# Kernel optimization log

Hardware: AMD Instinct MI355X
Metric: run time of the kernel (lower is better)

The kernel has to match this reference:

```python
import jax, jax.numpy as jnp
import numpy as np

B = 16384          # batch
F = 26             # num sparse features
D = 13             # num dense features
V = 100000         # vocab per sparse feature
E = 16             # embedding size
HID = [400, 400, 400]
DNN_IN = F * E + D  # 429


def setup_inputs() -> dict:
    key = jax.random.key(0)
    ks = jax.random.split(key, 16)
    inp = {}
    inp["x_sparse"] = jax.random.randint(ks[0], (B, F), 0, V, dtype=jnp.int32)
    inp["x_dense"] = jax.random.uniform(ks[1], (B, D), dtype=jnp.float32)
    # embedding tables (stacked across features; all vocabs equal)
    inp["emb1"] = jax.random.normal(ks[2], (F, V, 1), dtype=jnp.float32) * 0.0001
    inp["emb2"] = jax.random.normal(ks[3], (F, V, E), dtype=jnp.float32) * 0.0001
    inp["w_dense"] = jax.random.normal(ks[4], (D, 1), dtype=jnp.float32) * 0.0001
    inp["bias"] = jnp.zeros((1,), dtype=jnp.float32)
    dims = [DNN_IN] + HID
    for i in range(3):
        inp[f"dnn_w{i}"] = jax.random.normal(ks[5 + i], (dims[i], dims[i + 1]), dtype=jnp.float32) * 0.02
        inp[f"dnn_b{i}"] = jnp.zeros((dims[i + 1],), dtype=jnp.float32)
    inp["final_w"] = jax.random.normal(ks[9], (HID[-1], 1), dtype=jnp.float32) * 0.02
    return inp


def reference(x_sparse, x_dense, emb1, emb2, w_dense, bias,
              dnn_w0, dnn_b0, dnn_w1, dnn_b1, dnn_w2, dnn_b2, final_w):
    f_idx = jnp.arange(F)[None, :]                      # [1, F]
    # FM linear: per-feature 1-d embedding lookup, summed over features
    e1 = emb1[f_idx, x_sparse, 0]                       # [B, F]
    linear_sparse = jnp.sum(e1, axis=-1, keepdims=True)  # [B, 1]
    linear_dense = x_dense @ w_dense                    # [B, 1]
    logit = linear_sparse + linear_dense
    # FM second order: square-of-sum minus sum-of-square
    fm = emb2[f_idx, x_sparse]                          # [B, F, E]
    s = jnp.sum(fm, axis=1)                             # [B, E]
    cross = 0.5 * jnp.sum(s * s - jnp.sum(fm * fm, axis=1), axis=-1, keepdims=True)  # [B, 1]
    logit = logit + cross
    # DNN
    h = jnp.concatenate([fm.reshape(x_sparse.shape[0], F * E), x_dense], axis=-1)  # [B, F*E+D]
    h = jax.nn.relu(h @ dnn_w0 + dnn_b0)
    h = jax.nn.relu(h @ dnn_w1 + dnn_b1)
    h = jax.nn.relu(h @ dnn_w2 + dnn_b2)
    logit = logit + h @ final_w                         # [B, 1]
    return jax.nn.sigmoid(logit + bias)
```

## Files before the change

kernel.cpp:

```cpp
#include <hip/hip_runtime.h>
#include <hip/hip_bf16.h>
#include <math.h>

#define BATCH 16384
#define NF 26
#define ND 13
#define VOC 100000
#define KP0 448
#define KP1 416
#define CS 80
#define NSL 5
#define NGB 4096

typedef __bf16 bf16x8 __attribute__((ext_vector_type(8)));
typedef float f32x4 __attribute__((ext_vector_type(4)));
using bf16 = __hip_bfloat16;
typedef unsigned short u16;

__device__ __forceinline__ void gload_lds16(const void* g, void* l) {
  __builtin_amdgcn_global_load_lds(
      (const __attribute__((address_space(1))) void*)g,
      (__attribute__((address_space(3))) void*)l, 16, 0, 0);
}

__device__ __forceinline__ u16 f2bu(float v) {
  union { __hip_bfloat16 b; u16 u; } cv;
  cv.b = __float2bfloat16(v);
  return cv.u;
}

__global__ __launch_bounds__(256) void prep_gather_kernel(
    const float* __restrict__ w0, const float* __restrict__ w1,
    const float* __restrict__ w2, bf16* __restrict__ wt0,
    bf16* __restrict__ wt1, bf16* __restrict__ wt2,
    const int* __restrict__ xs, const float* __restrict__ xd,
    const float* __restrict__ emb1, const float* __restrict__ emb2,
    const float* __restrict__ wd, const float* __restrict__ biasp,
    bf16* __restrict__ h0, float* __restrict__ partial) {
  const int bid = blockIdx.x, tid = threadIdx.x;
  if (bid >= NGB) {
    const int pbid = bid - NGB;
    const float* W; bf16* Wt; int K, KP, idx;
    if (pbid < 728)       { W = w0; Wt = wt0; K = 429; KP = KP0; idx = pbid * 256 + tid; }
    else if (pbid < 1404) { W = w1; Wt = wt1; K = 400; KP = KP1; idx = (pbid - 728) * 256 + tid; }
    else                  { W = w2; Wt = wt2; K = 400; KP = KP1; idx = (pbid - 1404) * 256 + tid; }
    int k = idx % KP, n = idx / KP;
    float v = (k < K && n < 400) ? W[(size_t)k * 400 + n] : 0.f;
    Wt[idx] = __float2bfloat16(v);
    return;
  }
  const int p = bid;
  const int x8 = p & 7, qb = p >> 3;
  const int gl = (qb >> 5) * 256 + x8 * 32 + (qb & 31);
  const int w = tid >> 6, lane = tid & 63;
  const int b = gl * 4 + w;
  const int q = lane >> 2, sub = lane & 3;

  int xsl = 0;
  if (lane < NF) xsl = xs[b * NF + lane];
  float lin = 0.f;
  if (lane < NF) lin = emb1[(size_t)lane * VOC + xsl];
  if (lane < ND) lin += xd[b * ND + lane] * wd[lane];

  float4 sv = make_float4(0.f, 0.f, 0.f, 0.f);
  float sq = 0.f;
#pragma unroll
  for (int i = 0; i < 2; ++i) {
    int f = i * 16 + q;
    if (f < NF) {
      int idx = __shfl(xsl, f);
      float4 v = *((const float4*)(emb2 + ((size_t)f * VOC + idx) * 16) + sub);
      sv.x += v.x; sv.y += v.y; sv.z += v.z; sv.w += v.w;
      sq += v.x * v.x + v.y * v.y + v.z * v.z + v.w * v.w;
      ushort4 st;
      st.x = f2bu(v.x); st.y = f2bu(v.y); st.z = f2bu(v.z); st.w = f2bu(v.w);
      *(ushort4*)(h0 + (size_t)b * KP0 + f * 16 + sub * 4) = st;
    }
  }
  if (lane < 32) {
    float v = (lane < ND) ? xd[b * ND + lane] : 0.f;
    h0[(size_t)b * KP0 + 416 + lane] = __float2bfloat16(v);
  }
#pragma unroll
  for (int off = 4; off < 64; off <<= 1) {
    sv.x += __shfl_xor(sv.x, off);
    sv.y += __shfl_xor(sv.y, off);
    sv.z += __shfl_xor(sv.z, off);
    sv.w += __shfl_xor(sv.w, off);
  }
  float t = sv.x * sv.x + sv.y * sv.y + sv.z * sv.z + sv.w * sv.w;
#pragma unroll
  for (int off = 1; off < 64; off <<= 1) {
    t += __shfl_xor(t, off);
    sq += __shfl_xor(sq, off);
    lin += __shfl_xor(lin, off);
  }
  if (lane == 0)
    partial[b] = biasp[0] + lin + 0.5f * (t * 0.0625f - sq);
}

template <int NK, bool FINAL>
__global__ __launch_bounds__(256, 2) void gemm_kernel(
    const bf16* __restrict__ A, const bf16* __restrict__ Wt,
    const float* __restrict__ bias, bf16* __restrict__ outH,
    const float* __restrict__ fw, float* __restrict__ dotb) {
  constexpr int KP = NK * 32;
  extern __shared__ __align__(16) char smem[];
  const int b = blockIdx.x, tid = threadIdx.x;
  const int w = tid >> 6, lane = tid & 63, r = lane & 15, g = lane >> 4;
  const int lane8 = b & 7, hi = b >> 3;
  const int s = hi % NSL, mchunk = (hi / NSL) * 8 + lane8;
  const int row0 = mchunk * 128, col0 = s * CS;

  const char* Ab = (const char*)(A + (size_t)(row0 + w * 32 + r) * KP) + g * 16;
  const size_t rtS = (size_t)16 * KP * 2;
  bf16x8 a0[NK], a1[NK];
#pragma unroll
  for (int k = 0; k < NK; ++k) {
    a0[k] = *(const bf16x8*)(Ab + k * 64);
    a1[k] = *(const bf16x8*)(Ab + k * 64 + rtS);
  }

  {
    const char* wbase = (const char*)(Wt + (size_t)col0 * KP);
    constexpr int T = NK * CS * 4;
    constexpr int FULL = T >> 8, REM = T & 255;
    for (int rd = 0; rd <= FULL; ++rd) {
      if (rd < FULL || tid < REM) {
        int c = rd * 256 + tid;
        int kk = c / (CS * 4), rm = c - kk * (CS * 4);
        int n = rm >> 2, j = rm & 3;
        int kc = j ^ ((n >> 1) & 3);
        gload_lds16(wbase + (size_t)n * (KP * 2) + kk * 64 + kc * 16,
                    smem + (rd * 256 + w * 64) * 16);
      }
    }
  }
  __syncthreads();

  f32x4 acc[2][NSL];
#pragma unroll
  for (int rt = 0; rt < 2; ++rt)
#pragma unroll
    for (int ct = 0; ct < NSL; ++ct) acc[rt][ct] = (f32x4){0.f, 0.f, 0.f, 0.f};

  const int swz = ((g ^ ((r >> 1) & 3)) << 4);
#pragma unroll
  for (int k = 0; k < NK; ++k) {
    const char* sb = smem + k * (CS * 64) + r * 64 + swz;
#pragma unroll
    for (int ct = 0; ct < NSL; ++ct) {
      bf16x8 bfr = *(const bf16x8*)(sb + ct * 1024);
      acc[0][ct] = __builtin_amdgcn_mfma_f32_16x16x32_bf16(a0[k], bfr, acc[0][ct], 0, 0, 0);
      acc[1][ct] = __builtin_amdgcn_mfma_f32_16x16x32_bf16(a1[k], bfr, acc[1][ct], 0, 0, 0);
    }
  }

  if (!FINAL) {
#pragma unroll
    for (int ct = 0; ct < NSL; ++ct) {
      int col = col0 + ct * 16 + r;
      float bv = bias[col];
#pragma unroll
      for (int rt = 0; rt < 2; ++rt)
#pragma unroll
        for (int q = 0; q < 4; ++q) {
          float v = fmaxf(acc[rt][ct][q] + bv, 0.f);
          outH[(size_t)(row0 + w * 32 + rt * 16 + g * 4 + q) * KP1 + col] =
              __float2bfloat16(v);
        }
    }
  } else {
    float pr[2][4] = {{0.f, 0.f, 0.f, 0.f}, {0.f, 0.f, 0.f, 0.f}};
#pragma unroll
    for (int ct = 0; ct < NSL; ++ct) {
      int col = col0 + ct * 16 + r;
      float bv = bias[col], fv = fw[col];
#pragma unroll
      for (int rt = 0; rt < 2; ++rt)
#pragma unroll
        for (int q = 0; q < 4; ++q)
          pr[rt][q] += fmaxf(acc[rt][ct][q] + bv, 0.f) * fv;
    }
#pragma unroll
    for (int rt = 0; rt < 2; ++rt)
#pragma unroll
      for (int q = 0; q < 4; ++q) {
        pr[rt][q] += __shfl_xor(pr[rt][q], 1);
        pr[rt][q] += __shfl_xor(pr[rt][q], 2);
        pr[rt][q] += __shfl_xor(pr[rt][q], 4);
        pr[rt][q] += __shfl_xor(pr[rt][q], 8);
      }
    if (r < 4) {
#pragma unroll
      for (int rt = 0; rt < 2; ++rt) {
        float v = (r == 0) ? pr[rt][0] : (r == 1) ? pr[rt][1]
                : (r == 2) ? pr[rt][2] : pr[rt][3];
        dotb[(size_t)s * BATCH + row0 + w * 32 + rt * 16 + g * 4 + r] = v;
      }
    }
  }
}

__global__ void finish_kernel(const float* __restrict__ partial,
                              const float* __restrict__ dotb,
                              float* __restrict__ out) {
  int i = blockIdx.x * 256 + threadIdx.x;
  if (i < BATCH) {
    float x = partial[i] + dotb[i] + dotb[BATCH + i] + dotb[2 * BATCH + i]
            + dotb[3 * BATCH + i] + dotb[4 * BATCH + i];
    out[i] = 1.f / (1.f + expf(-x));
  }
}

extern "C" void kernel_launch(void* const* d_in, const int* in_sizes, int n_in,
                              void* d_out, int out_size, void* d_ws, size_t ws_size,
                              hipStream_t stream) {
  const int* xs = (const int*)d_in[0];
  const float* xd = (const float*)d_in[1];
  const float* emb1 = (const float*)d_in[2];
  const float* emb2 = (const float*)d_in[3];
  const float* wd = (const float*)d_in[4];
  const float* bias = (const float*)d_in[5];
  const float* w0 = (const float*)d_in[6];
  const float* b0 = (const float*)d_in[7];
  const float* w1 = (const float*)d_in[8];
  const float* b1 = (const float*)d_in[9];
  const float* w2 = (const float*)d_in[10];
  const float* b2 = (const float*)d_in[11];
  const float* fw = (const float*)d_in[12];
  float* out = (float*)d_out;

  char* ws = (char*)d_ws;
  float* partial = (float*)(ws + 0);
  float* dotb    = (float*)(ws + 65536);
  bf16* wt0 = (bf16*)(ws + 393216);
  bf16* wt1 = (bf16*)(ws + 765952);
  bf16* wt2 = (bf16*)(ws + 1112064);
  bf16* h0  = (bf16*)(ws + 1458176);
  bf16* h1  = (bf16*)(ws + 16138240);
  bf16* h2  = (bf16*)(ws + 29769728);

  constexpr int LDS14 = 14 * CS * 64;
  constexpr int LDS13 = 13 * CS * 64;
  hipFuncSetAttribute((const void*)gemm_kernel<14, false>,
                      hipFuncAttributeMaxDynamicSharedMemorySize, LDS14);
  hipFuncSetAttribute((const void*)gemm_kernel<13, false>,
                      hipFuncAttributeMaxDynamicSharedMemorySize, LDS13);
  hipFuncSetAttribute((const void*)gemm_kernel<13, true>,
                      hipFuncAttributeMaxDynamicSharedMemorySize, LDS13);

  prep_gather_kernel<<<NGB + 2080, 256, 0, stream>>>(
      w0, w1, w2, wt0, wt1, wt2, xs, xd, emb1, emb2, wd, bias, h0, partial);

  gemm_kernel<14, false><<<640, 256, LDS14, stream>>>(h0, wt0, b0, h1, nullptr, nullptr);
  gemm_kernel<13, false><<<640, 256, LDS13, stream>>>(h1, wt1, b1, h2, nullptr, nullptr);
  gemm_kernel<13, true><<<640, 256, LDS13, stream>>>(h2, wt2, b2, nullptr, fw, dotb);

  finish_kernel<<<64, 256, 0, stream>>>(partial, dotb, out);
}
```

Before: 70.78 us.

## Widen GEMM column slice to 112 and stage weights in two K halves

The GEMM kernels now split the 400 output columns into 4 slices of 112 instead of 5 slices of 80. This reduces the grid from 640 to 512 blocks and cuts redundant A-tile loads per row chunk. Weight tiles are staged into LDS in two K halves that reuse one 7-chunk buffer, with a barrier in between, to keep LDS per block within budget. The transposed weight padding grows to 448 columns and the epilogue masks columns past 400. In exchange, padded columns do wasted MFMA work, each block holds more accumulator registers, and the extra barrier and restaging add serialization.

After: 64.95 us, median of 3. 1.09x faster.

```diff
diff --git a/kernel.cpp b/kernel.cpp
--- a/kernel.cpp
+++ b/kernel.cpp
@@ -8,9 +8,10 @@
 #define VOC 100000
 #define KP0 448
 #define KP1 416
-#define CS 80
-#define NSL 5
+#define CS 112
+#define NSL 4
 #define NGB 4096
+#define NPB 2240
 
 typedef __bf16 bf16x8 __attribute__((ext_vector_type(8)));
 typedef float f32x4 __attribute__((ext_vector_type(4)));
@@ -41,9 +42,9 @@
   if (bid >= NGB) {
     const int pbid = bid - NGB;
     const float* W; bf16* Wt; int K, KP, idx;
-    if (pbid < 728)       { W = w0; Wt = wt0; K = 429; KP = KP0; idx = pbid * 256 + tid; }
-    else if (pbid < 1404) { W = w1; Wt = wt1; K = 400; KP = KP1; idx = (pbid - 728) * 256 + tid; }
-    else                  { W = w2; Wt = wt2; K = 400; KP = KP1; idx = (pbid - 1404) * 256 + tid; }
+    if (pbid < 784)       { W = w0; Wt = wt0; K = 429; KP = KP0; idx = pbid * 256 + tid; }
+    else if (pbid < 1512) { W = w1; Wt = wt1; K = 400; KP = KP1; idx = (pbid - 784) * 256 + tid; }
+    else                  { W = w2; Wt = wt2; K = 400; KP = KP1; idx = (pbid - 1512) * 256 + tid; }
     int k = idx % KP, n = idx / KP;
     float v = (k < K && n < 400) ? W[(size_t)k * 400 + n] : 0.f;
     Wt[idx] = __float2bfloat16(v);
@@ -105,82 +106,108 @@
     const float* __restrict__ bias, bf16* __restrict__ outH,
     const float* __restrict__ fw, float* __restrict__ dotb) {
   constexpr int KP = NK * 32;
+  constexpr int NKB = NK - 7;
   extern __shared__ __align__(16) char smem[];
   const int b = blockIdx.x, tid = threadIdx.x;
   const int w = tid >> 6, lane = tid & 63, r = lane & 15, g = lane >> 4;
   const int lane8 = b & 7, hi = b >> 3;
-  const int s = hi % NSL, mchunk = (hi / NSL) * 8 + lane8;
+  const int s = hi & 3, mchunk = (hi >> 2) * 8 + lane8;
   const int row0 = mchunk * 128, col0 = s * CS;
+  const char* wbase = (const char*)(Wt + (size_t)col0 * KP);
+
+  auto stageP = [&](int kbase, int chunks) {
+    for (int c0 = 0; c0 < chunks; c0 += 256) {
+      int c = c0 + tid;
+      if (c < chunks) {
+        int kk = c / (CS * 4);
+        int rm = c - kk * (CS * 4);
+        int n = rm >> 2, j = rm & 3;
+        int kc = j ^ ((n >> 1) & 3);
+        gload_lds16(wbase + (size_t)n * (KP * 2) + (kbase + kk) * 64 + kc * 16,
+                    smem + (c0 + w * 64) * 16);
+      }
+    }
+  };
 
   const char* Ab = (const char*)(A + (size_t)(row0 + w * 32 + r) * KP) + g * 16;
   const size_t rtS = (size_t)16 * KP * 2;
-  bf16x8 a0[NK], a1[NK];
-#pragma unroll
-  for (int k = 0; k < NK; ++k) {
-    a0[k] = *(const bf16x8*)(Ab + k * 64);
-    a1[k] = *(const bf16x8*)(Ab + k * 64 + rtS);
-  }
-
-  {
-    const char* wbase = (const char*)(Wt + (size_t)col0 * KP);
-    constexpr int T = NK * CS * 4;
-    constexpr int FULL = T >> 8, REM = T & 255;
-    for (int rd = 0; rd <= FULL; ++rd) {
-      if (rd < FULL || tid < REM) {
-        int c = rd * 256 + tid;
-        int kk = c / (CS * 4), rm = c - kk * (CS * 4);
-        int n = rm >> 2, j = rm & 3;
-        int kc = j ^ ((n >> 1) & 3);
-        gload_lds16(wbase + (size_t)n * (KP * 2) + kk * 64 + kc * 16,
-                    smem + (rd * 256 + w * 64) * 16);
-      }
-    }
-  }
+
+  bf16x8 aA0[7], aA1[7];
+#pragma unroll
+  for (int k = 0; k < 7; ++k) {
+    aA0[k] = *(const bf16x8*)(Ab + k * 64);
+    aA1[k] = *(const bf16x8*)(Ab + k * 64 + rtS);
+  }
+  stageP(0, 7 * CS * 4);
   __syncthreads();
 
-  f32x4 acc[2][NSL];
+  bf16x8 aB0[NKB], aB1[NKB];
+#pragma unroll
+  for (int k = 0; k < NKB; ++k) {
+    aB0[k] = *(const bf16x8*)(Ab + (7 + k) * 64);
+    aB1[k] = *(const bf16x8*)(Ab + (7 + k) * 64 + rtS);
+  }
+
+  f32x4 acc[2][7];
 #pragma unroll
   for (int rt = 0; rt < 2; ++rt)
 #pragma unroll
-    for (int ct = 0; ct < NSL; ++ct) acc[rt][ct] = (f32x4){0.f, 0.f, 0.f, 0.f};
+    for (int ct = 0; ct < 7; ++ct) acc[rt][ct] = (f32x4){0.f, 0.f, 0.f, 0.f};
 
   const int swz = ((g ^ ((r >> 1) & 3)) << 4);
 #pragma unroll
-  for (int k = 0; k < NK; ++k) {
-    const char* sb = smem + k * (CS * 64) + r * 64 + swz;
-#pragma unroll
-    for (int ct = 0; ct < NSL; ++ct) {
+  for (int kk = 0; kk < 7; ++kk) {
+    const char* sb = smem + kk * (CS * 64) + r * 64 + swz;
+#pragma unroll
+    for (int ct = 0; ct < 7; ++ct) {
       bf16x8 bfr = *(const bf16x8*)(sb + ct * 1024);
-      acc[0][ct] = __builtin_amdgcn_mfma_f32_16x16x32_bf16(a0[k], bfr, acc[0][ct], 0, 0, 0);
-      acc[1][ct] = __builtin_amdgcn_mfma_f32_16x16x32_bf16(a1[k], bfr, acc[1][ct], 0, 0, 0);
+      acc[0][ct] = __builtin_amdgcn_mfma_f32_16x16x32_bf16(aA0[kk], bfr, acc[0][ct], 0, 0, 0);
+      acc[1][ct] = __builtin_amdgcn_mfma_f32_16x16x32_bf16(aA1[kk], bfr, acc[1][ct], 0, 0, 0);
+    }
+  }
+  __syncthreads();
+  stageP(7, NKB * CS * 4);
+  __syncthreads();
+#pragma unroll
+  for (int kk = 0; kk < NKB; ++kk) {
+    const char* sb = smem + kk * (CS * 64) + r * 64 + swz;
+#pragma unroll
+    for (int ct = 0; ct < 7; ++ct) {
+      bf16x8 bfr = *(const bf16x8*)(sb + ct * 1024);
+      acc[0][ct] = __builtin_amdgcn_mfma_f32_16x16x32_bf16(aB0[kk], bfr, acc[0][ct], 0, 0, 0);
+      acc[1][ct] = __builtin_amdgcn_mfma_f32_16x16x32_bf16(aB1[kk], bfr, acc[1][ct], 0, 0, 0);
     }
   }
 
   if (!FINAL) {
 #pragma unroll
-    for (int ct = 0; ct < NSL; ++ct) {
+    for (int ct = 0; ct < 7; ++ct) {
       int col = col0 + ct * 16 + r;
-      float bv = bias[col];
-#pragma unroll
-      for (int rt = 0; rt < 2; ++rt)
-#pragma unroll
-        for (int q = 0; q < 4; ++q) {
-          float v = fmaxf(acc[rt][ct][q] + bv, 0.f);
-          outH[(size_t)(row0 + w * 32 + rt * 16 + g * 4 + q) * KP1 + col] =
-              __float2bfloat16(v);
-        }
+      if (col < 400) {
+        float bv = bias[col];
+#pragma unroll
+        for (int rt = 0; rt < 2; ++rt)
+#pragma unroll
+          for (int q = 0; q < 4; ++q) {
+            float v = fmaxf(acc[rt][ct][q] + bv, 0.f);
+            outH[(size_t)(row0 + w * 32 + rt * 16 + g * 4 + q) * KP1 + col] =
+                __float2bfloat16(v);
+          }
+      }
     }
   } else {
     float pr[2][4] = {{0.f, 0.f, 0.f, 0.f}, {0.f, 0.f, 0.f, 0.f}};
 #pragma unroll
-    for (int ct = 0; ct < NSL; ++ct) {
+    for (int ct = 0; ct < 7; ++ct) {
       int col = col0 + ct * 16 + r;
-      float bv = bias[col], fv = fw[col];
-#pragma unroll
-      for (int rt = 0; rt < 2; ++rt)
-#pragma unroll
-        for (int q = 0; q < 4; ++q)
-          pr[rt][q] += fmaxf(acc[rt][ct][q] + bv, 0.f) * fv;
+      if (col < 400) {
+        float bv = bias[col], fv = fw[col];
+#pragma unroll
+        for (int rt = 0; rt < 2; ++rt)
+#pragma unroll
+          for (int q = 0; q < 4; ++q)
+            pr[rt][q] += fmaxf(acc[rt][ct][q] + bv, 0.f) * fv;
+      }
     }
 #pragma unroll
     for (int rt = 0; rt < 2; ++rt)
@@ -208,7 +235,7 @@
   int i = blockIdx.x * 256 + threadIdx.x;
   if (i < BATCH) {
     float x = partial[i] + dotb[i] + dotb[BATCH + i] + dotb[2 * BATCH + i]
-            + dotb[3 * BATCH + i] + dotb[4 * BATCH + i];
+            + dotb[3 * BATCH + i];
     out[i] = 1.f / (1.f + expf(-x));
   }
 }
@@ -234,28 +261,27 @@
   char* ws = (char*)d_ws;
   float* partial = (float*)(ws + 0);
   float* dotb    = (float*)(ws + 65536);
-  bf16* wt0 = (bf16*)(ws + 393216);
-  bf16* wt1 = (bf16*)(ws + 765952);
-  bf16* wt2 = (bf16*)(ws + 1112064);
-  bf16* h0  = (bf16*)(ws + 1458176);
-  bf16* h1  = (bf16*)(ws + 16138240);
-  bf16* h2  = (bf16*)(ws + 29769728);
-
-  constexpr int LDS14 = 14 * CS * 64;
-  constexpr int LDS13 = 13 * CS * 64;
+  bf16* wt0 = (bf16*)(ws + 327680);
+  bf16* wt1 = (bf16*)(ws + 729088);
+  bf16* wt2 = (bf16*)(ws + 1101824);
+  bf16* h0  = (bf16*)(ws + 1474560);
+  bf16* h1  = (bf16*)(ws + 16154624);
+  bf16* h2  = (bf16*)(ws + 29786112);
+
+  constexpr int LDSB = 7 * CS * 64;
   hipFuncSetAttribute((const void*)gemm_kernel<14, false>,
-                      hipFuncAttributeMaxDynamicSharedMemorySize, LDS14);
+                      hipFuncAttributeMaxDynamicSharedMemorySize, LDSB);
   hipFuncSetAttribute((const void*)gemm_kernel<13, false>,
-                      hipFuncAttributeMaxDynamicSharedMemorySize, LDS13);
+                      hipFuncAttributeMaxDynamicSharedMemorySize, LDSB);
   hipFuncSetAttribute((const void*)gemm_kernel<13, true>,
-                      hipFuncAttributeMaxDynamicSharedMemorySize, LDS13);
-
-  prep_gather_kernel<<<NGB + 2080, 256, 0, stream>>>(
+                      hipFuncAttributeMaxDynamicSharedMemorySize, LDSB);
+
+  prep_gather_kernel<<<NGB + NPB, 256, 0, stream>>>(
       w0, w1, w2, wt0, wt1, wt2, xs, xd, emb1, emb2, wd, bias, h0, partial);
 
-  gemm_kernel<14, false><<<640, 256, LDS14, stream>>>(h0, wt0, b0, h1, nullptr, nullptr);
-  gemm_kernel<13, false><<<640, 256, LDS13, stream>>>(h1, wt1, b1, h2, nullptr, nullptr);
-  gemm_kernel<13, true><<<640, 256, LDS13, stream>>>(h2, wt2, b2, nullptr, fw, dotb);
+  gemm_kernel<14, false><<<512, 256, LDSB, stream>>>(h0, wt0, b0, h1, nullptr, nullptr);
+  gemm_kernel<13, false><<<512, 256, LDSB, stream>>>(h1, wt1, b1, h2, nullptr, nullptr);
+  gemm_kernel<13, true><<<512, 256, LDSB, stream>>>(h2, wt2, b2, nullptr, fw, dotb);
 
   finish_kernel<<<64, 256, 0, stream>>>(partial, dotb, out);
 }
```
